# Kernel optimization log

Hardware: AMD Instinct MI355X
Metric: run time of the kernel (lower is better)

Reference implementation:

```python
import jax, jax.numpy as jnp
import numpy as np

EMBED_DIM = 1024
NUM_HEADS = 16
HEAD_DIM = EMBED_DIM // NUM_HEADS


def setup_inputs() -> dict:
    key = jax.random.key(0)
    ks = jax.random.split(key, 6)
    B, S, D = 2, 2048, EMBED_DIM
    scale = 1.0 / np.sqrt(D)
    return {
        "inputs": jax.random.normal(ks[0], (B, S, D), dtype=jnp.float32),
        "Wq": jax.random.normal(ks[1], (D, D), dtype=jnp.float32) * scale,
        "Wk": jax.random.normal(ks[2], (D, D), dtype=jnp.float32) * scale,
        "Wv": jax.random.normal(ks[3], (D, D), dtype=jnp.float32) * scale,
        "Wo": jax.random.normal(ks[4], (D, D), dtype=jnp.float32) * scale,
        "bo": jnp.zeros((D,), dtype=jnp.float32),
    }


def reference(inputs, Wq, Wk, Wv, Wo, bo):
    B, S, D = inputs.shape
    H, P = NUM_HEADS, HEAD_DIM
    # torch Linear: x @ W.T ; weights stored [out, in]
    q = inputs @ Wq.T
    k = inputs @ Wk.T
    v = inputs @ Wv.T
    # separate heads: [B, S, H, P] -> [B, H, S, P]
    q = q.reshape(B, S, H, P).transpose(0, 2, 1, 3)
    k = k.reshape(B, S, H, P).transpose(0, 2, 1, 3)
    v = v.reshape(B, S, H, P).transpose(0, 2, 1, 3)
    # scaled dot-product attention; scale = 1/sqrt(P + 1e-9)
    scale = 1.0 / jnp.sqrt(jnp.float32(P) + 1e-9)
    scores = jnp.einsum("bhsp,bhtp->bhst", q, k) * scale
    weights = jax.nn.softmax(scores, axis=-1)
    attn = jnp.einsum("bhst,bhtp->bhsp", weights, v)
    # merge heads -> [B, S, D]
    concat = attn.transpose(0, 2, 1, 3).reshape(B, S, D)
    return concat @ Wo.T + bo
```

## Files before the change

kernel.cpp:

```cpp
#include <hip/hip_runtime.h>
#include <hip/hip_bf16.h>

typedef __bf16 bf16;
typedef __bf16 bf16x4 __attribute__((ext_vector_type(4)));
typedef __bf16 bf16x8 __attribute__((ext_vector_type(8)));
typedef short  s16x4  __attribute__((ext_vector_type(4)));
typedef float  f32x4  __attribute__((ext_vector_type(4)));

#define QSCALE 0.18033688011112042f

__device__ __forceinline__ float exp2_raw(float x) {
    return __builtin_amdgcn_exp2f(x);
}

__device__ __forceinline__ void load16_lds(const bf16* g, bf16* l) {
    __builtin_amdgcn_global_load_lds(
        (const __attribute__((address_space(1))) unsigned int*)g,
        (__attribute__((address_space(3))) unsigned int*)l, 16, 0, 0);
}

__global__ void cvt_f32_bf16(
    const float* __restrict__ s0, const float* __restrict__ s1,
    const float* __restrict__ s2, const float* __restrict__ s3,
    const float* __restrict__ s4,
    bf16* __restrict__ d0, bf16* __restrict__ d1, bf16* __restrict__ d2,
    bf16* __restrict__ d3, bf16* __restrict__ d4)
{
    int blk = blockIdx.x;
    const float* s; bf16* d; int off;
    if (blk < 2048) {
        s = s0; d = d0; off = blk;
    } else {
        int t = (blk - 2048) >> 9;
        off   = (blk - 2048) & 511;
        switch (t) {
            case 0:  s = s1; d = d1; break;
            case 1:  s = s2; d = d2; break;
            case 2:  s = s3; d = d3; break;
            default: s = s4; d = d4; break;
        }
    }
    int idx = off * 256 + threadIdx.x;
    float4 a = ((const float4*)s)[idx * 2];
    float4 b = ((const float4*)s)[idx * 2 + 1];
    bf16x8 o;
    o[0] = (bf16)a.x; o[1] = (bf16)a.y; o[2] = (bf16)a.z; o[3] = (bf16)a.w;
    o[4] = (bf16)b.x; o[5] = (bf16)b.y; o[6] = (bf16)b.z; o[7] = (bf16)b.w;
    *(bf16x8*)&d[idx * 8] = o;
}

__global__ __launch_bounds__(256, 3) void qkv_gemm(
    const bf16* __restrict__ A,
    const bf16* __restrict__ Wq, const bf16* __restrict__ Wk,
    const bf16* __restrict__ Wv,
    bf16* __restrict__ qbuf, bf16* __restrict__ kbuf, bf16* __restrict__ vT)
{
    __shared__ bf16 sA[128 * 64];
    __shared__ bf16 sB[128 * 64];

    const int hwflat = blockIdx.y * 24 + blockIdx.x;
    const int xcd    = hwflat & 7;
    const int slot   = hwflat >> 3;
    const int my     = xcd * 4 + slot / 24;
    const int mx     = slot % 24;

    const int which = mx >> 3;
    const int n0    = (mx & 7) * 128;
    const int m0    = my * 128;
    const bf16* B   = (which == 0) ? Wq : (which == 1) ? Wk : Wv;

    const int tid  = threadIdx.x;
    const int lane = tid & 63;
    const int w    = tid >> 6;
    const int wr   = w >> 1, wc = w & 1;
    const int r    = lane & 15;
    const int qd   = lane >> 4;

    f32x4 acc[4][4];
    const f32x4 zero4 = {0.f, 0.f, 0.f, 0.f};
#pragma unroll
    for (int mi = 0; mi < 4; ++mi)
#pragma unroll
        for (int ni = 0; ni < 4; ++ni) acc[mi][ni] = zero4;

    for (int kt = 0; kt < 16; ++kt) {
        const bf16* gA = A + (size_t)m0 * 1024 + kt * 64;
        const bf16* gB = B + (size_t)n0 * 1024 + kt * 64;
        __syncthreads();
#pragma unroll
        for (int j = 0; j < 4; ++j) {
            int flat = j * 256 + tid;
            int row  = flat >> 3, ch = flat & 7;
            int gc   = ((ch ^ (row & 7)) * 8);
            int ldsb = (j * 256 + w * 64) * 8;
            load16_lds(gA + (size_t)row * 1024 + gc, &sA[ldsb]);
            load16_lds(gB + (size_t)row * 1024 + gc, &sB[ldsb]);
        }
        __syncthreads();

#pragma unroll
        for (int ks = 0; ks < 2; ++ks) {
            bf16x8 af[4], bfr[4];
#pragma unroll
            for (int mi = 0; mi < 4; ++mi) {
                int row = wr * 64 + mi * 16 + r;
                af[mi] = *(const bf16x8*)&sA[row * 64 + (((ks * 4 + qd) ^ (r & 7)) * 8)];
            }
#pragma unroll
            for (int ni = 0; ni < 4; ++ni) {
                int row = wc * 64 + ni * 16 + r;
                bfr[ni] = *(const bf16x8*)&sB[row * 64 + (((ks * 4 + qd) ^ (r & 7)) * 8)];
            }
#pragma unroll
            for (int mi = 0; mi < 4; ++mi)
#pragma unroll
                for (int ni = 0; ni < 4; ++ni)
                    acc[mi][ni] = __builtin_amdgcn_mfma_f32_16x16x32_bf16(
                        af[mi], bfr[ni], acc[mi][ni], 0, 0, 0);
        }
    }

    const float scale = (which == 0) ? QSCALE : 1.0f;
#pragma unroll
    for (int mi = 0; mi < 4; ++mi)
#pragma unroll
        for (int ni = 0; ni < 4; ++ni) {
            int rb  = m0 + wr * 64 + mi * 16 + qd * 4;
            int col = n0 + wc * 64 + ni * 16 + r;
            if (which == 2) {
                bf16x4 pv;
#pragma unroll
                for (int i = 0; i < 4; ++i) pv[i] = (bf16)acc[mi][ni][i];
                *(bf16x4*)&vT[((size_t)((rb >> 11) * 1024 + col)) * 2048 + (rb & 2047)] = pv;
            } else {
                bf16* dst = (which == 0) ? qbuf : kbuf;
#pragma unroll
                for (int i = 0; i < 4; ++i)
                    dst[(size_t)(rb + i) * 1024 + col] = (bf16)(acc[mi][ni][i] * scale);
            }
        }
}

__global__ __launch_bounds__(256, 3) void out_gemm(
    const bf16* __restrict__ A, const bf16* __restrict__ B,
    float* __restrict__ C, const float* __restrict__ bias)
{
    __shared__ bf16 sA[128 * 64];
    __shared__ bf16 sB[64 * 64];

    const int hwflat = blockIdx.y * 16 + blockIdx.x;
    const int xcd    = hwflat & 7;
    const int slot   = hwflat >> 3;
    const int m0     = (xcd * 4 + (slot >> 4)) * 128;
    const int n0     = (slot & 15) * 64;

    const int tid  = threadIdx.x;
    const int lane = tid & 63;
    const int w    = tid >> 6;
    const int wr   = w >> 1, wc = w & 1;
    const int r    = lane & 15;
    const int qd   = lane >> 4;

    f32x4 acc[4][2];
    const f32x4 zero4 = {0.f, 0.f, 0.f, 0.f};
#pragma unroll
    for (int mi = 0; mi < 4; ++mi)
#pragma unroll
        for (int ni = 0; ni < 2; ++ni) acc[mi][ni] = zero4;

    for (int kt = 0; kt < 16; ++kt) {
        const bf16* gA = A + (size_t)m0 * 1024 + kt * 64;
        const bf16* gB = B + (size_t)n0 * 1024 + kt * 64;
        __syncthreads();
#pragma unroll
        for (int j = 0; j < 4; ++j) {
            int flat = j * 256 + tid;
            int row  = flat >> 3, ch = flat & 7;
            int gc   = ((ch ^ (row & 7)) * 8);
            int ldsb = (j * 256 + w * 64) * 8;
            load16_lds(gA + (size_t)row * 1024 + gc, &sA[ldsb]);
        }
#pragma unroll
        for (int j = 0; j < 2; ++j) {
            int flat = j * 256 + tid;
            int row  = flat >> 3, ch = flat & 7;
            int gc   = ((ch ^ (row & 7)) * 8);
            int ldsb = (j * 256 + w * 64) * 8;
            load16_lds(gB + (size_t)row * 1024 + gc, &sB[ldsb]);
        }
        __syncthreads();

#pragma unroll
        for (int ks = 0; ks < 2; ++ks) {
            bf16x8 af[4], bfr[2];
#pragma unroll
            for (int mi = 0; mi < 4; ++mi) {
                int row = wr * 64 + mi * 16 + r;
                af[mi] = *(const bf16x8*)&sA[row * 64 + (((ks * 4 + qd) ^ (r & 7)) * 8)];
            }
#pragma unroll
            for (int ni = 0; ni < 2; ++ni) {
                int row = wc * 32 + ni * 16 + r;
                bfr[ni] = *(const bf16x8*)&sB[row * 64 + (((ks * 4 + qd) ^ (r & 7)) * 8)];
            }
#pragma unroll
            for (int mi = 0; mi < 4; ++mi)
#pragma unroll
                for (int ni = 0; ni < 2; ++ni)
                    acc[mi][ni] = __builtin_amdgcn_mfma_f32_16x16x32_bf16(
                        af[mi], bfr[ni], acc[mi][ni], 0, 0, 0);
        }
    }

#pragma unroll
    for (int mi = 0; mi < 4; ++mi)
#pragma unroll
        for (int ni = 0; ni < 2; ++ni)
#pragma unroll
            for (int i = 0; i < 4; ++i) {
                int row = m0 + wr * 64 + mi * 16 + qd * 4 + i;
                int col = n0 + wc * 32 + ni * 16 + r;
                C[(size_t)row * 1024 + col] = acc[mi][ni][i] + bias[col];
            }
}

__global__ __launch_bounds__(512, 4) void attn_kernel(
    const bf16* __restrict__ qbuf, const bf16* __restrict__ kbuf,
    const bf16* __restrict__ vT, bf16* __restrict__ concat)
{
    __shared__ bf16 sKV[8 * 64 * 72];

    const int tid  = threadIdx.x;
    const int lane = tid & 63;
    const int w    = tid >> 6;
    const int g    = w >> 2;
    const int wq   = w & 3;
    const int gtid = tid & 255;
    const int r    = lane & 15;
    const int qd   = lane >> 4;

    const int hwflat = blockIdx.y * 16 + blockIdx.x;
    const int xcd    = hwflat & 7;
    const int slot   = hwflat >> 3;
    const int bh     = xcd * 4 + (slot >> 4);
    const int qt     = slot & 15;

    const int b    = bh >> 4, h = bh & 15;
    const int qrow0 = b * 2048 + qt * 128;
    const size_t vbase = (size_t)bh * 64 * 2048;

    const s16x4 ones4 = {(short)0x3F80, (short)0x3F80, (short)0x3F80, (short)0x3F80};

    int krow[2], kch[2];
#pragma unroll
    for (int t = 0; t < 2; ++t) {
        int flat = t * 256 + gtid;
        krow[t] = flat >> 3; kch[t] = flat & 7;
    }

    bf16x8 aq[2][2];
#pragma unroll
    for (int mi = 0; mi < 2; ++mi)
#pragma unroll
        for (int ks = 0; ks < 2; ++ks)
            aq[mi][ks] = *(const bf16x8*)&qbuf[
                (size_t)(qrow0 + wq * 32 + mi * 16 + r) * 1024 + h * 64 + ks * 32 + qd * 8];

    f32x4 acc_o[2][4], acc_l[2];
    const f32x4 zero4 = {0.f, 0.f, 0.f, 0.f};
#pragma unroll
    for (int mi = 0; mi < 2; ++mi) {
        acc_l[mi] = zero4;
#pragma unroll
        for (int pj = 0; pj < 4; ++pj) acc_o[mi][pj] = zero4;
    }

    bf16* const myKV = &sKV[g * 4 * 4608];

    bf16x8 rk[2], rv[2];
#pragma unroll
    for (int t = 0; t < 2; ++t) {
        rk[t] = *(const bf16x8*)&kbuf[(size_t)(b * 2048 + g * 64 + krow[t]) * 1024 + h * 64 + kch[t] * 8];
        rv[t] = *(const bf16x8*)&vT[vbase + (size_t)krow[t] * 2048 + g * 64 + kch[t] * 8];
    }
#pragma unroll
    for (int t = 0; t < 2; ++t) {
        *(bf16x8*)&myKV[0 * 4608 + krow[t] * 72 + kch[t] * 8] = rk[t];
        *(bf16x8*)&myKV[1 * 4608 + krow[t] * 72 + kch[t] * 8] = rv[t];
    }
#pragma unroll
    for (int t = 0; t < 2; ++t) {
        rk[t] = *(const bf16x8*)&kbuf[(size_t)(b * 2048 + (2 + g) * 64 + krow[t]) * 1024 + h * 64 + kch[t] * 8];
        rv[t] = *(const bf16x8*)&vT[vbase + (size_t)krow[t] * 2048 + (2 + g) * 64 + kch[t] * 8];
    }
    __syncthreads();

    for (int tt = 0; tt < 16; ++tt) {
        {
            int st = (tt + 1) & 1;
#pragma unroll
            for (int t = 0; t < 2; ++t) {
                *(bf16x8*)&myKV[(2 * st + 0) * 4608 + krow[t] * 72 + kch[t] * 8] = rk[t];
                *(bf16x8*)&myKV[(2 * st + 1) * 4608 + krow[t] * 72 + kch[t] * 8] = rv[t];
            }
        }
        {
            int nxtl = (tt + 2 < 16) ? tt + 2 : 15;
            int gt   = 2 * nxtl + g;
#pragma unroll
            for (int t = 0; t < 2; ++t) {
                rk[t] = *(const bf16x8*)&kbuf[(size_t)(b * 2048 + gt * 64 + krow[t]) * 1024 + h * 64 + kch[t] * 8];
                rv[t] = *(const bf16x8*)&vT[vbase + (size_t)krow[t] * 2048 + gt * 64 + kch[t] * 8];
            }
        }
        const bf16* sK = &myKV[(2 * (tt & 1) + 0) * 4608];
        const bf16* sV = &myKV[(2 * (tt & 1) + 1) * 4608];

        f32x4 accs[2][4];
#pragma unroll
        for (int mi = 0; mi < 2; ++mi)
#pragma unroll
            for (int ni = 0; ni < 4; ++ni) accs[mi][ni] = zero4;
        __builtin_amdgcn_s_setprio(1);
#pragma unroll
        for (int ks = 0; ks < 2; ++ks)
#pragma unroll
            for (int ni = 0; ni < 4; ++ni) {
                bf16x8 ak = *(const bf16x8*)&sK[(ni * 16 + r) * 72 + ks * 32 + qd * 8];
#pragma unroll
                for (int mi = 0; mi < 2; ++mi)
                    accs[mi][ni] = __builtin_amdgcn_mfma_f32_16x16x32_bf16(
                        ak, aq[mi][ks], accs[mi][ni], 0, 0, 0);
            }
        __builtin_amdgcn_s_setprio(0);

        s16x4 pfrag[2][4];
#pragma unroll
        for (int mi = 0; mi < 2; ++mi)
#pragma unroll
            for (int ni = 0; ni < 4; ++ni) {
                bf16x4 pv;
#pragma unroll
                for (int i = 0; i < 4; ++i) pv[i] = (bf16)exp2_raw(accs[mi][ni][i]);
                pfrag[mi][ni] = __builtin_bit_cast(s16x4, pv);
            }

        __builtin_amdgcn_s_setprio(1);
#pragma unroll
        for (int ni = 0; ni < 4; ++ni) {
#pragma unroll
            for (int pj = 0; pj < 4; ++pj) {
                bf16x4 av = *(const bf16x4*)&sV[(pj * 16 + r) * 72 + ni * 16 + qd * 4];
                s16x4  avs = __builtin_bit_cast(s16x4, av);
#pragma unroll
                for (int mi = 0; mi < 2; ++mi)
                    acc_o[mi][pj] = __builtin_amdgcn_mfma_f32_16x16x16bf16_1k(
                        avs, pfrag[mi][ni], acc_o[mi][pj], 0, 0, 0);
            }
#pragma unroll
            for (int mi = 0; mi < 2; ++mi)
                acc_l[mi] = __builtin_amdgcn_mfma_f32_16x16x16bf16_1k(
                    ones4, pfrag[mi][ni], acc_l[mi], 0, 0, 0);
        }
        __builtin_amdgcn_s_setprio(0);

        __syncthreads();
    }

    float* sF = (float*)sKV;
    bf16*  sO = sKV + 18432;

    if (g == 1) {
        int slotc = gtid * 35;
#pragma unroll
        for (int mi = 0; mi < 2; ++mi)
#pragma unroll
            for (int pj = 0; pj < 4; ++pj)
#pragma unroll
                for (int i = 0; i < 4; ++i)
                    sF[slotc + mi * 16 + pj * 4 + i] = acc_o[mi][pj][i];
        sF[slotc + 32] = acc_l[0][0];
        sF[slotc + 33] = acc_l[1][0];
    }
    __syncthreads();
    if (g == 0) {
        int slotc = gtid * 35;
        float inv[2];
#pragma unroll
        for (int mi = 0; mi < 2; ++mi)
            inv[mi] = 1.0f / (acc_l[mi][0] + sF[slotc + 32 + mi]);
#pragma unroll
        for (int mi = 0; mi < 2; ++mi) {
            int qloc = wq * 32 + mi * 16 + r;
#pragma unroll
            for (int pj = 0; pj < 4; ++pj)
#pragma unroll
                for (int i = 0; i < 4; ++i) {
                    float o = acc_o[mi][pj][i] + sF[slotc + mi * 16 + pj * 4 + i];
                    sO[qloc * 72 + pj * 16 + qd * 4 + i] = (bf16)(o * inv[mi]);
                }
        }
    }
    __syncthreads();
    {
        int row = tid >> 2;
        int q4  = tid & 3;
        size_t cb = (size_t)(qrow0 + row) * 1024 + h * 64 + q4 * 16;
        *(bf16x8*)&concat[cb]     = *(const bf16x8*)&sO[row * 72 + q4 * 16];
        *(bf16x8*)&concat[cb + 8] = *(const bf16x8*)&sO[row * 72 + q4 * 16 + 8];
    }
}

extern "C" void kernel_launch(void* const* d_in, const int* in_sizes, int n_in,
                              void* d_out, int out_size, void* d_ws, size_t ws_size,
                              hipStream_t stream)
{
    const float* x  = (const float*)d_in[0];
    const float* Wq = (const float*)d_in[1];
    const float* Wk = (const float*)d_in[2];
    const float* Wv = (const float*)d_in[3];
    const float* Wo = (const float*)d_in[4];
    const float* bo = (const float*)d_in[5];
    float* out = (float*)d_out;

    char* ws = (char*)d_ws;
    bf16* xb     = (bf16*)(ws);
    bf16* Wqb    = (bf16*)(ws + (8u  << 20));
    bf16* Wkb    = (bf16*)(ws + (10u << 20));
    bf16* Wvb    = (bf16*)(ws + (12u << 20));
    bf16* Wob    = (bf16*)(ws + (14u << 20));
    bf16* qbuf   = (bf16*)(ws + (16u << 20));
    bf16* kbuf   = (bf16*)(ws + (24u << 20));
    bf16* vT     = (bf16*)(ws + (32u << 20));
    bf16* concat = (bf16*)(ws + (40u << 20));

    hipLaunchKernelGGL(cvt_f32_bf16, dim3(4096), dim3(256), 0, stream,
                       x, Wq, Wk, Wv, Wo, xb, Wqb, Wkb, Wvb, Wob);
    hipLaunchKernelGGL(qkv_gemm, dim3(24, 32), dim3(256), 0, stream,
                       xb, Wqb, Wkb, Wvb, qbuf, kbuf, vT);
    hipLaunchKernelGGL(attn_kernel, dim3(16, 32), dim3(512), 0, stream,
                       qbuf, kbuf, vT, concat);
    hipLaunchKernelGGL(out_gemm, dim3(16, 32), dim3(256), 0, stream,
                       concat, Wob, out, bo);
}
```

Measured before the change: 186.7 us.

## Read K/V MFMA fragments directly from global memory instead of LDS staging

Removes the double-buffered LDS staging of K and V tiles and the per-iteration block barrier. Each wave now loads its MFMA operand fragments straight from global memory, relying on L1/L2 caching, which shrinks shared memory to what the epilogue reduction needs. The epilogue gains an extra barrier because the output staging buffer now aliases the reduction scratch. The cost is more redundant global/cache traffic, since the four waves in a group each reload the same K/V fragments, and the V reads are narrow 8-byte loads.

```diff
diff --git a/kernel.cpp b/kernel.cpp
--- a/kernel.cpp
+++ b/kernel.cpp
@@ -228,7 +228,7 @@
     const bf16* __restrict__ qbuf, const bf16* __restrict__ kbuf,
     const bf16* __restrict__ vT, bf16* __restrict__ concat)
 {
-    __shared__ bf16 sKV[8 * 64 * 72];
+    __shared__ bf16 sKV[18432];
 
     const int tid  = threadIdx.x;
     const int lane = tid & 63;
@@ -247,16 +247,11 @@
 
     const int b    = bh >> 4, h = bh & 15;
     const int qrow0 = b * 2048 + qt * 128;
-    const size_t vbase = (size_t)bh * 64 * 2048;
 
     const s16x4 ones4 = {(short)0x3F80, (short)0x3F80, (short)0x3F80, (short)0x3F80};
 
-    int krow[2], kch[2];
-#pragma unroll
-    for (int t = 0; t < 2; ++t) {
-        int flat = t * 256 + gtid;
-        krow[t] = flat >> 3; kch[t] = flat & 7;
-    }
+    const bf16* kb = kbuf + (size_t)(b * 2048 + r) * 1024 + h * 64 + qd * 8;
+    const bf16* vb = vT + (size_t)bh * 64 * 2048 + (size_t)r * 2048 + qd * 4;
 
     bf16x8 aq[2][2];
 #pragma unroll
@@ -275,46 +270,10 @@
         for (int pj = 0; pj < 4; ++pj) acc_o[mi][pj] = zero4;
     }
 
-    bf16* const myKV = &sKV[g * 4 * 4608];
-
-    bf16x8 rk[2], rv[2];
-#pragma unroll
-    for (int t = 0; t < 2; ++t) {
-        rk[t] = *(const bf16x8*)&kbuf[(size_t)(b * 2048 + g * 64 + krow[t]) * 1024 + h * 64 + kch[t] * 8];
-        rv[t] = *(const bf16x8*)&vT[vbase + (size_t)krow[t] * 2048 + g * 64 + kch[t] * 8];
-    }
-#pragma unroll
-    for (int t = 0; t < 2; ++t) {
-        *(bf16x8*)&myKV[0 * 4608 + krow[t] * 72 + kch[t] * 8] = rk[t];
-        *(bf16x8*)&myKV[1 * 4608 + krow[t] * 72 + kch[t] * 8] = rv[t];
-    }
-#pragma unroll
-    for (int t = 0; t < 2; ++t) {
-        rk[t] = *(const bf16x8*)&kbuf[(size_t)(b * 2048 + (2 + g) * 64 + krow[t]) * 1024 + h * 64 + kch[t] * 8];
-        rv[t] = *(const bf16x8*)&vT[vbase + (size_t)krow[t] * 2048 + (2 + g) * 64 + kch[t] * 8];
-    }
-    __syncthreads();
-
     for (int tt = 0; tt < 16; ++tt) {
-        {
-            int st = (tt + 1) & 1;
-#pragma unroll
-            for (int t = 0; t < 2; ++t) {
-                *(bf16x8*)&myKV[(2 * st + 0) * 4608 + krow[t] * 72 + kch[t] * 8] = rk[t];
-                *(bf16x8*)&myKV[(2 * st + 1) * 4608 + krow[t] * 72 + kch[t] * 8] = rv[t];
-            }
-        }
-        {
-            int nxtl = (tt + 2 < 16) ? tt + 2 : 15;
-            int gt   = 2 * nxtl + g;
-#pragma unroll
-            for (int t = 0; t < 2; ++t) {
-                rk[t] = *(const bf16x8*)&kbuf[(size_t)(b * 2048 + gt * 64 + krow[t]) * 1024 + h * 64 + kch[t] * 8];
-                rv[t] = *(const bf16x8*)&vT[vbase + (size_t)krow[t] * 2048 + gt * 64 + kch[t] * 8];
-            }
-        }
-        const bf16* sK = &myKV[(2 * (tt & 1) + 0) * 4608];
-        const bf16* sV = &myKV[(2 * (tt & 1) + 1) * 4608];
+        const int gt = 2 * tt + g;
+        const bf16* kt = kb + (size_t)gt * 64 * 1024;
+        const bf16* vt = vb + gt * 64;
 
         f32x4 accs[2][4];
 #pragma unroll
@@ -326,7 +285,7 @@
         for (int ks = 0; ks < 2; ++ks)
 #pragma unroll
             for (int ni = 0; ni < 4; ++ni) {
-                bf16x8 ak = *(const bf16x8*)&sK[(ni * 16 + r) * 72 + ks * 32 + qd * 8];
+                bf16x8 ak = *(const bf16x8*)&kt[(size_t)ni * 16 * 1024 + ks * 32];
 #pragma unroll
                 for (int mi = 0; mi < 2; ++mi)
                     accs[mi][ni] = __builtin_amdgcn_mfma_f32_16x16x32_bf16(
@@ -350,7 +309,7 @@
         for (int ni = 0; ni < 4; ++ni) {
 #pragma unroll
             for (int pj = 0; pj < 4; ++pj) {
-                bf16x4 av = *(const bf16x4*)&sV[(pj * 16 + r) * 72 + ni * 16 + qd * 4];
+                bf16x4 av = *(const bf16x4*)&vt[(size_t)pj * 16 * 2048 + ni * 16];
                 s16x4  avs = __builtin_bit_cast(s16x4, av);
 #pragma unroll
                 for (int mi = 0; mi < 2; ++mi)
@@ -363,12 +322,10 @@
                     ones4, pfrag[mi][ni], acc_l[mi], 0, 0, 0);
         }
         __builtin_amdgcn_s_setprio(0);
-
-        __syncthreads();
     }
 
     float* sF = (float*)sKV;
-    bf16*  sO = sKV + 18432;
+    bf16*  sO = sKV;
 
     if (g == 1) {
         int slotc = gtid * 35;
@@ -383,22 +340,31 @@
         sF[slotc + 33] = acc_l[1][0];
     }
     __syncthreads();
+    float inv0 = 0.f, inv1 = 0.f;
     if (g == 0) {
         int slotc = gtid * 35;
-        float inv[2];
+        inv0 = 1.0f / (acc_l[0][0] + sF[slotc + 32]);
+        inv1 = 1.0f / (acc_l[1][0] + sF[slotc + 33]);
 #pragma unroll
         for (int mi = 0; mi < 2; ++mi)
-            inv[mi] = 1.0f / (acc_l[mi][0] + sF[slotc + 32 + mi]);
+#pragma unroll
+            for (int pj = 0; pj < 4; ++pj)
+#pragma unroll
+                for (int i = 0; i < 4; ++i)
+                    acc_o[mi][pj][i] += sF[slotc + mi * 16 + pj * 4 + i];
+    }
+    __syncthreads();
+    if (g == 0) {
 #pragma unroll
         for (int mi = 0; mi < 2; ++mi) {
-            int qloc = wq * 32 + mi * 16 + r;
+            float inv = (mi == 0) ? inv0 : inv1;
+            int qloc  = wq * 32 + mi * 16 + r;
 #pragma unroll
             for (int pj = 0; pj < 4; ++pj)
 #pragma unroll
-                for (int i = 0; i < 4; ++i) {
-                    float o = acc_o[mi][pj][i] + sF[slotc + mi * 16 + pj * 4 + i];
-                    sO[qloc * 72 + pj * 16 + qd * 4 + i] = (bf16)(o * inv[mi]);
-                }
+                for (int i = 0; i < 4; ++i)
+                    sO[qloc * 72 + pj * 16 + qd * 4 + i] =
+                        (bf16)(acc_o[mi][pj][i] * inv);
         }
     }
     __syncthreads();
```

New measurement: 298.7 us. 60.0% more time.

## Stage V-transpose epilogue through LDS and swizzle attention K/V shared tiles

Applied to the files above, without the earlier changes.

The QKV GEMM epilogue for V now writes the accumulator tile transposed into shared memory (136-element padded rows, 34816 bytes of dynamic LDS) and then emits coalesced 16-byte rows into vT, replacing scattered 8-byte global stores. The attention kernel drops the 72-element padded K/V rows for 64-element rows with an XOR chunk swizzle, applied consistently on the stores and on the K and V fragment reads, which shrinks LDS use. The extra dynamic LDS in qkv_gemm may lower its occupancy. The prologue also issues a redundant first global load whose result is immediately overwritten.

```diff
diff --git a/kernel.cpp b/kernel.cpp
--- a/kernel.cpp
+++ b/kernel.cpp
@@ -55,8 +55,9 @@
     const bf16* __restrict__ Wv,
     bf16* __restrict__ qbuf, bf16* __restrict__ kbuf, bf16* __restrict__ vT)
 {
-    __shared__ bf16 sA[128 * 64];
-    __shared__ bf16 sB[128 * 64];
+    extern __shared__ bf16 smem[];
+    bf16* sA = smem;
+    bf16* sB = smem + 8192;
 
     const int hwflat = blockIdx.y * 24 + blockIdx.x;
     const int xcd    = hwflat & 7;
@@ -120,25 +121,48 @@
         }
     }
 
-    const float scale = (which == 0) ? QSCALE : 1.0f;
-#pragma unroll
-    for (int mi = 0; mi < 4; ++mi)
-#pragma unroll
-        for (int ni = 0; ni < 4; ++ni) {
-            int rb  = m0 + wr * 64 + mi * 16 + qd * 4;
-            int col = n0 + wc * 64 + ni * 16 + r;
-            if (which == 2) {
+    if (which == 2) {
+        bf16* sT = smem;
+        __syncthreads();
+#pragma unroll
+        for (int mi = 0; mi < 4; ++mi)
+#pragma unroll
+            for (int ni = 0; ni < 4; ++ni) {
+                int colL = wc * 64 + ni * 16 + r;
+                int sL   = wr * 64 + mi * 16 + qd * 4;
                 bf16x4 pv;
 #pragma unroll
                 for (int i = 0; i < 4; ++i) pv[i] = (bf16)acc[mi][ni][i];
-                *(bf16x4*)&vT[((size_t)((rb >> 11) * 1024 + col)) * 2048 + (rb & 2047)] = pv;
-            } else {
-                bf16* dst = (which == 0) ? qbuf : kbuf;
+                *(bf16x4*)&sT[colL * 136 + sL] = pv;
+            }
+        __syncthreads();
+        const int b0 = m0 >> 11, s0 = m0 & 2047;
+#pragma unroll
+        for (int rr = 0; rr < 2; ++rr) {
+            int colL = rr * 64 + (tid >> 2);
+            int q    = tid & 3;
+            bf16* dst = &vT[((size_t)(b0 * 1024 + n0 + colL)) * 2048 + s0];
+            const bf16* src = &sT[colL * 136];
+#pragma unroll
+            for (int c = 0; c < 4; ++c) {
+                bf16x8 v = *(const bf16x8*)&src[c * 32 + q * 8];
+                *(bf16x8*)&dst[c * 32 + q * 8] = v;
+            }
+        }
+    } else {
+        const float scale = (which == 0) ? QSCALE : 1.0f;
+        bf16* dst = (which == 0) ? qbuf : kbuf;
+#pragma unroll
+        for (int mi = 0; mi < 4; ++mi)
+#pragma unroll
+            for (int ni = 0; ni < 4; ++ni) {
+                int rb  = m0 + wr * 64 + mi * 16 + qd * 4;
+                int col = n0 + wc * 64 + ni * 16 + r;
 #pragma unroll
                 for (int i = 0; i < 4; ++i)
                     dst[(size_t)(rb + i) * 1024 + col] = (bf16)(acc[mi][ni][i] * scale);
             }
-        }
+    }
 }
 
 __global__ __launch_bounds__(256, 3) void out_gemm(
@@ -228,7 +252,7 @@
     const bf16* __restrict__ qbuf, const bf16* __restrict__ kbuf,
     const bf16* __restrict__ vT, bf16* __restrict__ concat)
 {
-    __shared__ bf16 sKV[8 * 64 * 72];
+    __shared__ bf16 sKV[8 * 64 * 64];
 
     const int tid  = threadIdx.x;
     const int lane = tid & 63;
@@ -251,11 +275,12 @@
 
     const s16x4 ones4 = {(short)0x3F80, (short)0x3F80, (short)0x3F80, (short)0x3F80};
 
-    int krow[2], kch[2];
+    int krow[2], kchS[2];
 #pragma unroll
     for (int t = 0; t < 2; ++t) {
         int flat = t * 256 + gtid;
-        krow[t] = flat >> 3; kch[t] = flat & 7;
+        krow[t] = flat >> 3;
+        kchS[t] = (flat & 7) ^ (krow[t] & 7);
     }
 
     bf16x8 aq[2][2];
@@ -275,23 +300,32 @@
         for (int pj = 0; pj < 4; ++pj) acc_o[mi][pj] = zero4;
     }
 
-    bf16* const myKV = &sKV[g * 4 * 4608];
+    bf16* const myKV = &sKV[g * 4 * 4096];
 
     bf16x8 rk[2], rv[2];
 #pragma unroll
     for (int t = 0; t < 2; ++t) {
-        rk[t] = *(const bf16x8*)&kbuf[(size_t)(b * 2048 + g * 64 + krow[t]) * 1024 + h * 64 + kch[t] * 8];
-        rv[t] = *(const bf16x8*)&vT[vbase + (size_t)krow[t] * 2048 + g * 64 + kch[t] * 8];
+        rk[t] = *(const bf16x8*)&kbuf[(size_t)(b * 2048 + g * 64 + krow[t]) * 1024 + h * 64 + (t * 256 + gtid & 7) * 8];
+        rv[t] = *(const bf16x8*)&vT[vbase + (size_t)krow[t] * 2048 + g * 64 + ((t * 256 + gtid) & 7) * 8];
     }
 #pragma unroll
     for (int t = 0; t < 2; ++t) {
-        *(bf16x8*)&myKV[0 * 4608 + krow[t] * 72 + kch[t] * 8] = rk[t];
-        *(bf16x8*)&myKV[1 * 4608 + krow[t] * 72 + kch[t] * 8] = rv[t];
+        int flat = t * 256 + gtid;
+        int chL  = flat & 7;
+        rk[t] = *(const bf16x8*)&kbuf[(size_t)(b * 2048 + g * 64 + krow[t]) * 1024 + h * 64 + chL * 8];
+        rv[t] = *(const bf16x8*)&vT[vbase + (size_t)krow[t] * 2048 + g * 64 + chL * 8];
     }
 #pragma unroll
     for (int t = 0; t < 2; ++t) {
-        rk[t] = *(const bf16x8*)&kbuf[(size_t)(b * 2048 + (2 + g) * 64 + krow[t]) * 1024 + h * 64 + kch[t] * 8];
-        rv[t] = *(const bf16x8*)&vT[vbase + (size_t)krow[t] * 2048 + (2 + g) * 64 + kch[t] * 8];
+        *(bf16x8*)&myKV[0 * 4096 + krow[t] * 64 + kchS[t] * 8] = rk[t];
+        *(bf16x8*)&myKV[1 * 4096 + krow[t] * 64 + kchS[t] * 8] = rv[t];
+    }
+#pragma unroll
+    for (int t = 0; t < 2; ++t) {
+        int flat = t * 256 + gtid;
+        int chL  = flat & 7;
+        rk[t] = *(const bf16x8*)&kbuf[(size_t)(b * 2048 + (2 + g) * 64 + krow[t]) * 1024 + h * 64 + chL * 8];
+        rv[t] = *(const bf16x8*)&vT[vbase + (size_t)krow[t] * 2048 + (2 + g) * 64 + chL * 8];
     }
     __syncthreads();
 
@@ -300,8 +334,8 @@
             int st = (tt + 1) & 1;
 #pragma unroll
             for (int t = 0; t < 2; ++t) {
-                *(bf16x8*)&myKV[(2 * st + 0) * 4608 + krow[t] * 72 + kch[t] * 8] = rk[t];
-                *(bf16x8*)&myKV[(2 * st + 1) * 4608 + krow[t] * 72 + kch[t] * 8] = rv[t];
+                *(bf16x8*)&myKV[(2 * st + 0) * 4096 + krow[t] * 64 + kchS[t] * 8] = rk[t];
+                *(bf16x8*)&myKV[(2 * st + 1) * 4096 + krow[t] * 64 + kchS[t] * 8] = rv[t];
             }
         }
         {
@@ -309,12 +343,14 @@
             int gt   = 2 * nxtl + g;
 #pragma unroll
             for (int t = 0; t < 2; ++t) {
-                rk[t] = *(const bf16x8*)&kbuf[(size_t)(b * 2048 + gt * 64 + krow[t]) * 1024 + h * 64 + kch[t] * 8];
-                rv[t] = *(const bf16x8*)&vT[vbase + (size_t)krow[t] * 2048 + gt * 64 + kch[t] * 8];
-            }
-        }
-        const bf16* sK = &myKV[(2 * (tt & 1) + 0) * 4608];
-        const bf16* sV = &myKV[(2 * (tt & 1) + 1) * 4608];
+                int flat = t * 256 + gtid;
+                int chL  = flat & 7;
+                rk[t] = *(const bf16x8*)&kbuf[(size_t)(b * 2048 + gt * 64 + krow[t]) * 1024 + h * 64 + chL * 8];
+                rv[t] = *(const bf16x8*)&vT[vbase + (size_t)krow[t] * 2048 + gt * 64 + chL * 8];
+            }
+        }
+        const bf16* sK = &myKV[(2 * (tt & 1) + 0) * 4096];
+        const bf16* sV = &myKV[(2 * (tt & 1) + 1) * 4096];
 
         f32x4 accs[2][4];
 #pragma unroll
@@ -326,7 +362,7 @@
         for (int ks = 0; ks < 2; ++ks)
 #pragma unroll
             for (int ni = 0; ni < 4; ++ni) {
-                bf16x8 ak = *(const bf16x8*)&sK[(ni * 16 + r) * 72 + ks * 32 + qd * 8];
+                bf16x8 ak = *(const bf16x8*)&sK[(ni * 16 + r) * 64 + (((ks * 4 + qd) ^ (r & 7)) * 8)];
 #pragma unroll
                 for (int mi = 0; mi < 2; ++mi)
                     accs[mi][ni] = __builtin_amdgcn_mfma_f32_16x16x32_bf16(
@@ -350,7 +386,8 @@
         for (int ni = 0; ni < 4; ++ni) {
 #pragma unroll
             for (int pj = 0; pj < 4; ++pj) {
-                bf16x4 av = *(const bf16x4*)&sV[(pj * 16 + r) * 72 + ni * 16 + qd * 4];
+                int chV = ((ni * 2 + (qd >> 1)) ^ (r & 7)) * 8 + (qd & 1) * 4;
+                bf16x4 av = *(const bf16x4*)&sV[(pj * 16 + r) * 64 + chV];
                 s16x4  avs = __builtin_bit_cast(s16x4, av);
 #pragma unroll
                 for (int mi = 0; mi < 2; ++mi)
@@ -436,7 +473,7 @@
 
     hipLaunchKernelGGL(cvt_f32_bf16, dim3(4096), dim3(256), 0, stream,
                        x, Wq, Wk, Wv, Wo, xb, Wqb, Wkb, Wvb, Wob);
-    hipLaunchKernelGGL(qkv_gemm, dim3(24, 32), dim3(256), 0, stream,
+    hipLaunchKernelGGL(qkv_gemm, dim3(24, 32), dim3(256), 34816, stream,
                        xb, Wqb, Wkb, Wvb, qbuf, kbuf, vT);
     hipLaunchKernelGGL(attn_kernel, dim3(16, 32), dim3(512), 0, stream,
                        qbuf, kbuf, vT, concat);
```

Result: no change. 185.2 us (-0.8%).
